# Kernel tuning notes

Measured on AMD Instinct MI355X. Metric: run time of the kernel, lower is better.

## Reference

```python
import jax, jax.numpy as jnp
import numpy as np

EMBED_DIM = 2048
N_HEADS = 16
N_KV_HEADS = 4
HEAD_DIM = EMBED_DIM // N_HEADS  # 128
NUM_REP = N_HEADS // N_KV_HEADS  # 4
BATCH = 4
SEQLEN = 2048


def setup_inputs() -> dict:
    key = jax.random.key(0)
    kx, kq, kk, kv, ko = jax.random.split(key, 5)
    x = jax.random.normal(kx, (BATCH, SEQLEN, EMBED_DIM), dtype=jnp.float32)
    # Real RoPE table (theta=10000), shape (seqlen, head_dim//2)
    inv_freq = 1.0 / (10000.0 ** (jnp.arange(0, HEAD_DIM, 2, dtype=jnp.float32) / HEAD_DIM))
    t = jnp.arange(SEQLEN, dtype=jnp.float32)
    ang = jnp.outer(t, inv_freq)  # (S, hd/2)
    freqs_cos = jnp.cos(ang)
    freqs_sin = jnp.sin(ang)
    std = 0.02
    wq = jax.random.normal(kq, (EMBED_DIM, N_HEADS * HEAD_DIM), dtype=jnp.float32) * std
    wk = jax.random.normal(kk, (EMBED_DIM, N_KV_HEADS * HEAD_DIM), dtype=jnp.float32) * std
    wv = jax.random.normal(kv, (EMBED_DIM, N_KV_HEADS * HEAD_DIM), dtype=jnp.float32) * std
    wo = jax.random.normal(ko, (N_HEADS * HEAD_DIM, EMBED_DIM), dtype=jnp.float32) * std
    return {"x": x, "freqs_cos": freqs_cos, "freqs_sin": freqs_sin,
            "wq": wq, "wk": wk, "wv": wv, "wo": wo}


def _apply_rope(xh, cos, sin):
    # xh: (b, s, h, hd); cos/sin: (s, hd/2) -> broadcast (1, s, 1, hd/2)
    b, s, h, hd = xh.shape
    xr = xh.reshape(b, s, h, hd // 2, 2)
    x0, x1 = xr[..., 0], xr[..., 1]  # real/imag of complex pairs
    c = cos[None, :, None, :]
    sn = sin[None, :, None, :]
    o0 = x0 * c - x1 * sn
    o1 = x0 * sn + x1 * c
    return jnp.stack([o0, o1], axis=-1).reshape(b, s, h, hd)


def reference(x, freqs_cos, freqs_sin, wq, wk, wv, wo):
    bs, s, _ = x.shape
    xq = (x @ wq).reshape(bs, s, N_HEADS, HEAD_DIM)
    xk = (x @ wk).reshape(bs, s, N_KV_HEADS, HEAD_DIM)
    xv = (x @ wv).reshape(bs, s, N_KV_HEADS, HEAD_DIM)
    xq = _apply_rope(xq, freqs_cos, freqs_sin)
    xk = _apply_rope(xk, freqs_cos, freqs_sin)
    # repeat_kv (GQA): interleave-repeat kv heads to match query heads
    keys = jnp.repeat(xk, NUM_REP, axis=2)    # (b, s, H, hd)
    values = jnp.repeat(xv, NUM_REP, axis=2)
    scale = 1.0 / jnp.sqrt(jnp.float32(HEAD_DIM))
    # SDPA, non-causal
    scores = jnp.einsum('bqhd,bkhd->bhqk', xq, keys) * scale
    probs = jax.nn.softmax(scores, axis=-1)
    out = jnp.einsum('bhqk,bkhd->bqhd', probs, values)
    out = out.reshape(bs, s, N_HEADS * HEAD_DIM)
    return out @ wo
```

## Files before the change

### kernel.cpp

```cpp
#include <hip/hip_runtime.h>
#include <stdint.h>


typedef unsigned short u16;
typedef __bf16 bf16x8 __attribute__((ext_vector_type(8)));
typedef float  f32x4  __attribute__((ext_vector_type(4)));

#define GLOAD16(gp, lp)                                                        \
  __builtin_amdgcn_global_load_lds(                                            \
      (const __attribute__((address_space(1))) void*)(gp),                     \
      (__attribute__((address_space(3))) void*)(lp), 16, 0, 0)

__device__ __forceinline__ u16 f2b(float f) {
  union { float f; uint32_t u; } v; v.f = f;
  uint32_t r = v.u + 0x7FFFu + ((v.u >> 16) & 1u);
  return (u16)(r >> 16);
}
__device__ __forceinline__ float b2f(u16 h) {
  union { uint32_t u; float f; } v; v.u = ((uint32_t)h) << 16;
  return v.f;
}
__device__ __forceinline__ uint2 pack4(float a, float b, float c, float d) {
  uint2 r;
  asm("v_cvt_pk_bf16_f32 %0, %1, %2" : "=v"(r.x) : "v"(a), "v"(b));
  asm("v_cvt_pk_bf16_f32 %0, %1, %2" : "=v"(r.y) : "v"(c), "v"(d));
  return r;
}

__device__ __forceinline__ void bar_sync() {
  asm volatile("s_waitcnt lgkmcnt(0)" ::: "memory");
  __builtin_amdgcn_s_barrier();
  asm volatile("" ::: "memory");
}

__global__ __launch_bounds__(256) void cast_x_kernel(const float4* __restrict__ in,
                                                     ushort4* __restrict__ out) {
  int i = blockIdx.x * 256 + threadIdx.x;
  float4 v = in[i];
  ushort4 o;
  o.x = f2b(v.x); o.y = f2b(v.y); o.z = f2b(v.z); o.w = f2b(v.w);
  out[i] = o;
}

__global__ __launch_bounds__(256) void wtrans_kernel(const float* __restrict__ W,
                                                     u16* __restrict__ WT,
                                                     int K, int N, float scale) {
  __shared__ float t[32][33];
  int n0 = blockIdx.x * 32, k0 = blockIdx.y * 32;
  int tx = threadIdx.x, ty = threadIdx.y;
  for (int r = 0; r < 4; r++)
    t[ty + r * 8][tx] = W[(size_t)(k0 + ty + r * 8) * N + n0 + tx];
  __syncthreads();
  for (int r = 0; r < 4; r++)
    WT[(size_t)(n0 + ty + r * 8) * K + k0 + tx] = f2b(t[tx][ty + r * 8] * scale);
}

template <bool BF16OUT>
__global__ __launch_bounds__(256) void gemm_bt_kernel(const u16* __restrict__ A,
                                                      const u16* __restrict__ BT,
                                                      void* __restrict__ Cv,
                                                      int K, int N) {
  __shared__ u16 As[128 * 32];
  __shared__ u16 Bs[128 * 32];
  const int tid = threadIdx.x;
  const int wave = tid >> 6, lane = tid & 63;
  const int quad = lane >> 4, l16 = lane & 15;
  const int wm = (wave >> 1) * 64, wn = (wave & 1) * 64;
  const size_t m0 = (size_t)blockIdx.y * 128, n0 = (size_t)blockIdx.x * 128;

  f32x4 acc[4][4] = {};
  const int srow = lane >> 2;
  const int scol = (lane & 3) * 8;
  const u16* Ag = A + (m0 + wave * 16 + srow) * (size_t)K + scol;
  const u16* Bg = BT + (n0 + wave * 16 + srow) * (size_t)K + scol;

  for (int k0 = 0; k0 < K; k0 += 32) {
    for (int rd = 0; rd < 2; rd++) {
      GLOAD16(Ag + (size_t)rd * 64 * K + k0, &As[(rd * 64 + wave * 16) * 32]);
      GLOAD16(Bg + (size_t)rd * 64 * K + k0, &Bs[(rd * 64 + wave * 16) * 32]);
    }
    __syncthreads();
    bf16x8 af[4], bf[4];
    for (int i = 0; i < 4; i++)
      af[i] = *(const bf16x8*)&As[(wm + i * 16 + l16) * 32 + quad * 8];
    for (int i = 0; i < 4; i++)
      bf[i] = *(const bf16x8*)&Bs[(wn + i * 16 + l16) * 32 + quad * 8];
    for (int mi = 0; mi < 4; mi++)
      for (int ni = 0; ni < 4; ni++)
        acc[mi][ni] = __builtin_amdgcn_mfma_f32_16x16x32_bf16(af[mi], bf[ni], acc[mi][ni], 0, 0, 0);
    __syncthreads();
  }
  for (int mi = 0; mi < 4; mi++)
    for (int ni = 0; ni < 4; ni++)
      for (int r = 0; r < 4; r++) {
        size_t row = m0 + wm + mi * 16 + quad * 4 + r;
        size_t col = n0 + wn + ni * 16 + l16;
        if (BF16OUT) ((u16*)Cv)[row * N + col] = f2b(acc[mi][ni][r]);
        else         ((float*)Cv)[row * N + col] = acc[mi][ni][r];
      }
}

__global__ __launch_bounds__(256) void rope_kernel(u16* __restrict__ QKV,
                                                   const float* __restrict__ cs,
                                                   const float* __restrict__ sn) {
  int tid = blockIdx.x * 256 + threadIdx.x;
  int row = tid / 1280;
  int p = tid - row * 1280;
  int s = row & 2047;
  int head = p >> 6, i = p & 63;
  u16* ptr = QKV + (size_t)row * 3072 + head * 128 + i * 2;
  unsigned int v = *(unsigned int*)ptr;
  float x0 = b2f((u16)(v & 0xffff)), x1 = b2f((u16)(v >> 16));
  float c = cs[s * 64 + i], ss = sn[s * 64 + i];
  u16 o0 = f2b(x0 * c - x1 * ss);
  u16 o1 = f2b(x0 * ss + x1 * c);
  *(unsigned int*)ptr = (unsigned int)o0 | ((unsigned int)o1 << 16);
}

__global__ __launch_bounds__(256) void vtrans_kernel(const u16* __restrict__ QKV,
                                                     u16* __restrict__ Vt) {
  __shared__ u16 t[32][33];
  int b = blockIdx.z >> 2, hk = blockIdx.z & 3;
  int s0 = blockIdx.x * 32, d0 = blockIdx.y * 32;
  int tx = threadIdx.x, ty = threadIdx.y;
  const u16* src = QKV + (size_t)(b * 2048 + s0) * 3072 + 2560 + hk * 128 + d0;
  for (int r = 0; r < 4; r++)
    t[ty + r * 8][tx] = src[(size_t)(ty + r * 8) * 3072 + tx];
  __syncthreads();
  u16* dst = Vt + ((size_t)((b * 4 + hk) * 128 + d0)) * 2048 + s0;
  for (int r = 0; r < 4; r++)
    dst[(size_t)(ty + r * 8) * 2048 + tx] = t[tx][ty + r * 8];
}

__global__ __launch_bounds__(256, 2) void attn_kernel(const u16* __restrict__ QKV,
                                                      const u16* __restrict__ Vt,
                                                      u16* __restrict__ AO) {
  __shared__ u16 KP[128 * 128];
  __shared__ u16 Vls[128 * 128];
  const int tid = threadIdx.x;
  const int wave = tid >> 6, lane = tid & 63;
  const int quad = lane >> 4, l16 = lane & 15;
  const int qt = blockIdx.x, h = blockIdx.y, b = blockIdx.z;
  const int hk = h >> 2;
  const int sw = l16 & 7;

  bf16x8 qf[2][4];
  {
    const u16* Qb = QKV + (size_t)(b * 2048 + qt * 128 + wave * 32) * 3072 + h * 128;
    for (int qb = 0; qb < 2; qb++)
      for (int ki = 0; ki < 4; ki++)
        qf[qb][ki] = *(const bf16x8*)(Qb + (size_t)(qb * 16 + l16) * 3072 + ki * 32 + quad * 8);
  }
  f32x4 o[8][2] = {};
  float m_[2] = {-1e30f, -1e30f}, l_[2] = {0.f, 0.f};

  const u16* Kg0 = QKV + 2048 + hk * 128;
  const u16* Vg0 = Vt + (size_t)((b * 4 + hk) * 128) * 2048;
  const int r4 = lane >> 4, c16 = lane & 15;

  auto stageK = [&](int t) {
    const u16* Kg = Kg0 + (size_t)(b * 2048 + t * 128) * 3072;
    for (int i = 0; i < 8; i++) {
      int grp = i * 4 + wave;
      int row = grp * 4 + r4;
      int ch = c16 ^ (row & 7);
      GLOAD16(Kg + (size_t)row * 3072 + ch * 8, &KP[grp * 512]);
    }
  };
  auto stageV = [&](int t) {
    const u16* Vg = Vg0 + t * 128;
    for (int i = 0; i < 8; i++) {
      int grp = i * 4 + wave;
      int row = grp * 4 + r4;
      int ch = c16 ^ (row & 7);
      GLOAD16(Vg + (size_t)row * 2048 + ch * 8, &Vls[grp * 512]);
    }
  };

  stageK(0);
  stageV(0);
  __syncthreads();

  const int bpA = (((quad & 1) << 5) + l16) << 2;
  const int bpB = bpA + 64;
  const bool hi = quad >= 2;

  for (int kt = 0; kt < 16; kt++) {
    if (kt > 0) stageV(kt);

    f32x4 s[8][2];
    for (int kb = 0; kb < 8; kb++) {
      bf16x8 kf[4];
      int a0 = (kb * 16 + l16) * 128 + ((quad ^ sw) << 3);
      for (int ki = 0; ki < 4; ki++)
        kf[ki] = *(const bf16x8*)&KP[a0 ^ (ki * 32)];
      __builtin_amdgcn_s_setprio(1);
      for (int qb = 0; qb < 2; qb++) {
        f32x4 a = {0.f, 0.f, 0.f, 0.f};
        for (int ki = 0; ki < 4; ki++)
          a = __builtin_amdgcn_mfma_f32_16x16x32_bf16(kf[ki], qf[qb][ki], a, 0, 0, 0);
        s[kb][qb] = a;
      }
      __builtin_amdgcn_s_setprio(0);
    }

    bar_sync();
    if (kt < 15) stageK(kt + 1);

    bf16x8 pf[2][4];
    float alch[2];
    for (int qb = 0; qb < 2; qb++) {
      float mk[8];
#pragma unroll
      for (int kb = 0; kb < 8; kb++)
        mk[kb] = fmaxf(fmaxf(s[kb][qb][0], s[kb][qb][1]),
                       fmaxf(s[kb][qb][2], s[kb][qb][3]));
      float mx = fmaxf(fmaxf(fmaxf(mk[0], mk[1]), fmaxf(mk[2], mk[3])),
                       fmaxf(fmaxf(mk[4], mk[5]), fmaxf(mk[6], mk[7])));
      mx = fmaxf(mx, __shfl_xor(mx, 16, 64));
      mx = fmaxf(mx, __shfl_xor(mx, 32, 64));
      float mn = m_[qb], al = 1.0f;
      if (!__all(mx <= m_[qb] + 8.0f)) {
        mn = fmaxf(m_[qb], mx);
        al = exp2f(m_[qb] - mn);
        m_[qb] = mn;
      }
      alch[qb] = al;
      uint2 u[8];
      float rs = 0.f;
#pragma unroll
      for (int kb = 0; kb < 8; kb++) {
        float p0 = exp2f(s[kb][qb][0] - mn), p1 = exp2f(s[kb][qb][1] - mn);
        float p2 = exp2f(s[kb][qb][2] - mn), p3 = exp2f(s[kb][qb][3] - mn);
        u[kb] = pack4(p0, p1, p2, p3);
        rs += (p0 + p1) + (p2 + p3);
      }
      rs += __shfl_xor(rs, 16, 64);
      rs += __shfl_xor(rs, 32, 64);
      l_[qb] = l_[qb] * al + rs;
#pragma unroll
      for (int ki = 0; ki < 4; ki++) {
        int Ax = (int)u[2 * ki].x, Ay = (int)u[2 * ki].y;
        int Bx = (int)u[2 * ki + 1].x, By = (int)u[2 * ki + 1].y;
        int pAx = __builtin_amdgcn_ds_bpermute(bpA, Ax);
        int pBx = __builtin_amdgcn_ds_bpermute(bpA, Bx);
        int pAy = __builtin_amdgcn_ds_bpermute(bpA, Ay);
        int pBy = __builtin_amdgcn_ds_bpermute(bpA, By);
        int qAx = __builtin_amdgcn_ds_bpermute(bpB, Ax);
        int qBx = __builtin_amdgcn_ds_bpermute(bpB, Bx);
        int qAy = __builtin_amdgcn_ds_bpermute(bpB, Ay);
        int qBy = __builtin_amdgcn_ds_bpermute(bpB, By);
        uint4 d;
        d.x = hi ? (uint32_t)pBx : (uint32_t)pAx;
        d.y = hi ? (uint32_t)pBy : (uint32_t)pAy;
        d.z = hi ? (uint32_t)qBx : (uint32_t)qAx;
        d.w = hi ? (uint32_t)qBy : (uint32_t)qAy;
        pf[qb][ki] = *(bf16x8*)&d;
      }
    }
    if (alch[0] != 1.0f || alch[1] != 1.0f) {
#pragma unroll
      for (int db = 0; db < 8; db++) {
        o[db][0] *= alch[0];
        o[db][1] *= alch[1];
      }
    }

    if (kt == 15) asm volatile("s_waitcnt vmcnt(0)" ::: "memory");
    else          asm volatile("s_waitcnt vmcnt(8)" ::: "memory");
    bar_sync();

    for (int db = 0; db < 8; db++) {
      bf16x8 vf[4];
      int a0 = (db * 16 + l16) * 128 + ((quad ^ sw) << 3);
      for (int ki = 0; ki < 4; ki++)
        vf[ki] = *(const bf16x8*)&Vls[a0 ^ (ki * 32)];
      __builtin_amdgcn_s_setprio(1);
      for (int qb = 0; qb < 2; qb++)
        for (int ki = 0; ki < 4; ki++)
          o[db][qb] = __builtin_amdgcn_mfma_f32_16x16x32_bf16(vf[ki], pf[qb][ki], o[db][qb], 0, 0, 0);
      __builtin_amdgcn_s_setprio(0);
    }

    asm volatile("s_waitcnt vmcnt(0)" ::: "memory");
    bar_sync();
  }

  float inv[2] = {1.0f / l_[0], 1.0f / l_[1]};
  for (int qb = 0; qb < 2; qb++) {
    int rq = wave * 32 + qb * 16 + l16;
    for (int db = 0; db < 8; db++) {
      int ch = (db * 2 + (quad >> 1)) ^ sw;
      uint2 pv = pack4(o[db][qb][0] * inv[qb], o[db][qb][1] * inv[qb],
                       o[db][qb][2] * inv[qb], o[db][qb][3] * inv[qb]);
      *(uint2*)&KP[rq * 128 + (ch << 3) + (quad & 1) * 4] = pv;
    }
  }
  __syncthreads();
  u16* Ab = AO + (size_t)(b * 2048 + qt * 128) * 2048 + h * 128;
  for (int i = 0; i < 8; i++) {
    int row = i * 16 + (tid >> 4);
    int seg = tid & 15;
    int pc = seg ^ (row & 7);
    *(uint4*)(Ab + (size_t)row * 2048 + seg * 8) = *(const uint4*)&KP[row * 128 + pc * 8];
  }
}

extern "C" void kernel_launch(void* const* d_in, const int* in_sizes, int n_in,
                              void* d_out, int out_size, void* d_ws, size_t ws_size,
                              hipStream_t stream) {
  (void)in_sizes; (void)n_in; (void)out_size; (void)ws_size;
  const float* x    = (const float*)d_in[0];
  const float* fcos = (const float*)d_in[1];
  const float* fsin = (const float*)d_in[2];
  const float* wq   = (const float*)d_in[3];
  const float* wk   = (const float*)d_in[4];
  const float* wv   = (const float*)d_in[5];
  const float* wo   = (const float*)d_in[6];

  char* w = (char*)d_ws;
  u16* xb  = (u16*)w;
  u16* wT  = (u16*)(w + 33554432);
  u16* woT = (u16*)(w + 33554432 + 12582912);
  u16* QKV = (u16*)(w + 33554432 + 12582912 + 8388608);
  u16* Vt  = (u16*)(w + 33554432 + 12582912 + 8388608 + 50331648);
  u16* AO  = xb;

  const float C = 0.08838834764831845f * 1.44269504088896340f;

  cast_x_kernel<<<16384, 256, 0, stream>>>((const float4*)x, (ushort4*)xb);
  wtrans_kernel<<<dim3(64, 64), dim3(32, 8), 0, stream>>>(wq, wT, 2048, 2048, C);
  wtrans_kernel<<<dim3(16, 64), dim3(32, 8), 0, stream>>>(wk, wT + (size_t)2048 * 2048, 2048, 512, 1.0f);
  wtrans_kernel<<<dim3(16, 64), dim3(32, 8), 0, stream>>>(wv, wT + (size_t)2560 * 2048, 2048, 512, 1.0f);
  wtrans_kernel<<<dim3(64, 64), dim3(32, 8), 0, stream>>>(wo, woT, 2048, 2048, 1.0f);

  gemm_bt_kernel<true><<<dim3(24, 64), 256, 0, stream>>>(xb, wT, QKV, 2048, 3072);
  rope_kernel<<<40960, 256, 0, stream>>>(QKV, fcos, fsin);
  vtrans_kernel<<<dim3(64, 4, 16), dim3(32, 8), 0, stream>>>(QKV, Vt);
  attn_kernel<<<dim3(16, 16, 4), 256, 0, stream>>>(QKV, Vt, AO);
  gemm_bt_kernel<false><<<dim3(16, 64), 256, 0, stream>>>(AO, woT, (float*)d_out, 2048, 2048);
}
```

Measured before the change: 618.1 us.

## Deepen GEMM K tile with XOR-swizzled LDS and use permlane32 swap for P

The projection GEMM now stages a K-step of 64 per iteration instead of 32, with an XOR-swizzled LDS layout. This halves the barrier count and is meant to cut bank conflicts on fragment reads, at the cost of doubled LDS use per block. In the attention kernel, the P-matrix register reshuffle drops eight ds_bpermute ops per chunk. In their place it uses two v_permlane32_swap plus four 16-lane xor shuffles, cutting LDS-crossbar traffic in the softmax-to-PV handoff.

Result: faster. 575.7 us (-6.9%).

```diff
diff --git a/kernel.cpp b/kernel.cpp
--- a/kernel.cpp
+++ b/kernel.cpp
@@ -5,6 +5,7 @@
 typedef unsigned short u16;
 typedef __bf16 bf16x8 __attribute__((ext_vector_type(8)));
 typedef float  f32x4  __attribute__((ext_vector_type(4)));
+typedef unsigned int u32x2 __attribute__((ext_vector_type(2)));
 
 #define GLOAD16(gp, lp)                                                        \
   __builtin_amdgcn_global_load_lds(                                            \
@@ -60,8 +61,8 @@
                                                       const u16* __restrict__ BT,
                                                       void* __restrict__ Cv,
                                                       int K, int N) {
-  __shared__ u16 As[128 * 32];
-  __shared__ u16 Bs[128 * 32];
+  __shared__ u16 As[128 * 64];
+  __shared__ u16 Bs[128 * 64];
   const int tid = threadIdx.x;
   const int wave = tid >> 6, lane = tid & 63;
   const int quad = lane >> 4, l16 = lane & 15;
@@ -69,25 +70,29 @@
   const size_t m0 = (size_t)blockIdx.y * 128, n0 = (size_t)blockIdx.x * 128;
 
   f32x4 acc[4][4] = {};
-  const int srow = lane >> 2;
-  const int scol = (lane & 3) * 8;
-  const u16* Ag = A + (m0 + wave * 16 + srow) * (size_t)K + scol;
-  const u16* Bg = BT + (n0 + wave * 16 + srow) * (size_t)K + scol;
-
-  for (int k0 = 0; k0 < K; k0 += 32) {
-    for (int rd = 0; rd < 2; rd++) {
-      GLOAD16(Ag + (size_t)rd * 64 * K + k0, &As[(rd * 64 + wave * 16) * 32]);
-      GLOAD16(Bg + (size_t)rd * 64 * K + k0, &Bs[(rd * 64 + wave * 16) * 32]);
+  const int srow = lane >> 3;
+  const int scol = ((lane & 7) ^ srow) * 8;
+  const u16* Ag = A + (m0 + wave * 8 + srow) * (size_t)K + scol;
+  const u16* Bg = BT + (n0 + wave * 8 + srow) * (size_t)K + scol;
+  const int sw7 = l16 & 7;
+
+  for (int k0 = 0; k0 < K; k0 += 64) {
+    for (int c = 0; c < 4; c++) {
+      GLOAD16(Ag + (size_t)(c * 32) * K + k0, &As[(c * 32 + wave * 8) * 64]);
+      GLOAD16(Bg + (size_t)(c * 32) * K + k0, &Bs[(c * 32 + wave * 8) * 64]);
     }
     __syncthreads();
-    bf16x8 af[4], bf[4];
-    for (int i = 0; i < 4; i++)
-      af[i] = *(const bf16x8*)&As[(wm + i * 16 + l16) * 32 + quad * 8];
-    for (int i = 0; i < 4; i++)
-      bf[i] = *(const bf16x8*)&Bs[(wn + i * 16 + l16) * 32 + quad * 8];
-    for (int mi = 0; mi < 4; mi++)
-      for (int ni = 0; ni < 4; ni++)
-        acc[mi][ni] = __builtin_amdgcn_mfma_f32_16x16x32_bf16(af[mi], bf[ni], acc[mi][ni], 0, 0, 0);
+    for (int kk = 0; kk < 2; kk++) {
+      bf16x8 af[4], bf[4];
+      const int ch = ((4 * kk + quad) ^ sw7) << 3;
+      for (int i = 0; i < 4; i++)
+        af[i] = *(const bf16x8*)&As[(wm + i * 16 + l16) * 64 + ch];
+      for (int i = 0; i < 4; i++)
+        bf[i] = *(const bf16x8*)&Bs[(wn + i * 16 + l16) * 64 + ch];
+      for (int mi = 0; mi < 4; mi++)
+        for (int ni = 0; ni < 4; ni++)
+          acc[mi][ni] = __builtin_amdgcn_mfma_f32_16x16x32_bf16(af[mi], bf[ni], acc[mi][ni], 0, 0, 0);
+    }
     __syncthreads();
   }
   for (int mi = 0; mi < 4; mi++)
@@ -180,10 +185,6 @@
   stageK(0);
   stageV(0);
   __syncthreads();
-
-  const int bpA = (((quad & 1) << 5) + l16) << 2;
-  const int bpB = bpA + 64;
-  const bool hi = quad >= 2;
 
   for (int kt = 0; kt < 16; kt++) {
     if (kt > 0) stageV(kt);
@@ -238,23 +239,20 @@
       rs += __shfl_xor(rs, 16, 64);
       rs += __shfl_xor(rs, 32, 64);
       l_[qb] = l_[qb] * al + rs;
+      const bool qo = (quad & 1) != 0;
 #pragma unroll
       for (int ki = 0; ki < 4; ki++) {
-        int Ax = (int)u[2 * ki].x, Ay = (int)u[2 * ki].y;
-        int Bx = (int)u[2 * ki + 1].x, By = (int)u[2 * ki + 1].y;
-        int pAx = __builtin_amdgcn_ds_bpermute(bpA, Ax);
-        int pBx = __builtin_amdgcn_ds_bpermute(bpA, Bx);
-        int pAy = __builtin_amdgcn_ds_bpermute(bpA, Ay);
-        int pBy = __builtin_amdgcn_ds_bpermute(bpA, By);
-        int qAx = __builtin_amdgcn_ds_bpermute(bpB, Ax);
-        int qBx = __builtin_amdgcn_ds_bpermute(bpB, Bx);
-        int qAy = __builtin_amdgcn_ds_bpermute(bpB, Ay);
-        int qBy = __builtin_amdgcn_ds_bpermute(bpB, By);
+        u32x2 r1 = __builtin_amdgcn_permlane32_swap(u[2 * ki].x, u[2 * ki + 1].x, false, false);
+        u32x2 r2 = __builtin_amdgcn_permlane32_swap(u[2 * ki].y, u[2 * ki + 1].y, false, false);
+        uint32_t t1b = (uint32_t)__shfl_xor((int)r1[1], 16, 64);
+        uint32_t t1a = (uint32_t)__shfl_xor((int)r1[0], 16, 64);
+        uint32_t t2b = (uint32_t)__shfl_xor((int)r2[1], 16, 64);
+        uint32_t t2a = (uint32_t)__shfl_xor((int)r2[0], 16, 64);
         uint4 d;
-        d.x = hi ? (uint32_t)pBx : (uint32_t)pAx;
-        d.y = hi ? (uint32_t)pBy : (uint32_t)pAy;
-        d.z = hi ? (uint32_t)qBx : (uint32_t)qAx;
-        d.w = hi ? (uint32_t)qBy : (uint32_t)qAy;
+        d.x = qo ? t1b : (uint32_t)r1[0];
+        d.y = qo ? t2b : (uint32_t)r2[0];
+        d.z = qo ? (uint32_t)r1[1] : t1a;
+        d.w = qo ? (uint32_t)r2[1] : t2a;
         pf[qb][ki] = *(bf16x8*)&d;
       }
     }
```
